# Performance work log

Measured on AMD Instinct MI355X. Metric: run time of the kernel, lower is better.

## Reference

```python
import jax, jax.numpy as jnp
import numpy as np

D_MODEL = 1024
NUM_HEADS = 16
D_K = D_MODEL // NUM_HEADS


def setup_inputs() -> dict:
    key = jax.random.key(0)
    ks = jax.random.split(key, 5)
    s = 1.0 / np.sqrt(D_MODEL)
    return {
        "x": jax.random.normal(ks[0], (2, 2048, D_MODEL), dtype=jnp.float32),
        "Wq": jax.random.normal(ks[1], (D_MODEL, D_MODEL), dtype=jnp.float32) * s,
        "bq": jnp.zeros((D_MODEL,), dtype=jnp.float32),
        "Wk": jax.random.normal(ks[2], (D_MODEL, D_MODEL), dtype=jnp.float32) * s,
        "bk": jnp.zeros((D_MODEL,), dtype=jnp.float32),
        "Wv": jax.random.normal(ks[3], (D_MODEL, D_MODEL), dtype=jnp.float32) * s,
        "bv": jnp.zeros((D_MODEL,), dtype=jnp.float32),
        "Wo": jax.random.normal(ks[4], (D_MODEL, D_MODEL), dtype=jnp.float32) * s,
        "bo": jnp.zeros((D_MODEL,), dtype=jnp.float32),
    }


def reference(x, Wq, bq, Wk, bk, Wv, bv, Wo, bo):
    B, S, D = x.shape
    H, dk = NUM_HEADS, D_K
    Q = x @ Wq + bq  # [B, S, D]
    K = x @ Wk + bk
    V = x @ Wv + bv
    # Faithful to the torch code: plain .view(B, H, S, dk) (NO transpose),
    # i.e. heads are carved out of the flattened (S*D) dim, not the feature dim.
    Q = Q.reshape(B, H, S, dk)
    K = K.reshape(B, H, S, dk)
    V = V.reshape(B, H, S, dk)
    scores = jnp.einsum("bhqd,bhkd->bhqk", Q, K) / jnp.sqrt(jnp.float32(dk))
    attn = jax.nn.softmax(scores, axis=-1)  # [B, H, S, S]
    ctx = jnp.einsum("bhqk,bhkd->bhqd", attn, V)  # [B, H, S, dk]
    out = ctx.reshape(B, S, D) @ Wo + bo
    return out  # dropout is identity in eval mode
```

## Files before the change

kernel.cpp:

```cpp
#include <hip/hip_runtime.h>
#include <hip/hip_bf16.h>
#include <math.h>

#define D_MODEL 1024
#define SEQ     2048
#define BATCH   2
#define NHEAD   16
#define DKH     64
#define BH      (BATCH * NHEAD)

typedef unsigned short u16;
typedef unsigned int   u32;
typedef __bf16 bf16x8 __attribute__((ext_vector_type(8)));
typedef float  f32x4  __attribute__((ext_vector_type(4)));

#define MFMA16(a, b, c) __builtin_amdgcn_mfma_f32_16x16x32_bf16((a), (b), (c), 0, 0, 0)
#define AS1 __attribute__((address_space(1)))
#define AS3 __attribute__((address_space(3)))

#define QSCALE 0.18033688f

__device__ __forceinline__ u16 f2bf(float x) {
    u32 u = __float_as_uint(x);
    u += 0x7fffu + ((u >> 16) & 1u);
    return (u16)(u >> 16);
}
__device__ __forceinline__ float bf2f(u16 b) {
    return __uint_as_float(((u32)b) << 16);
}
__device__ __forceinline__ void gl16(const u16* g, void* lds) {
    __builtin_amdgcn_global_load_lds((const AS1 u32*)g, (AS3 u32*)lds, 16, 0, 0);
}

__global__ __launch_bounds__(256) void conv_all(
    const float* __restrict__ x, u16* __restrict__ Xh, int n4,
    const float* __restrict__ W0, const float* __restrict__ W1,
    const float* __restrict__ W2, const float* __restrict__ W3,
    u16* __restrict__ H0, u16* __restrict__ L0, u16* __restrict__ H1, u16* __restrict__ L1,
    u16* __restrict__ H2, u16* __restrict__ L2, u16* __restrict__ H3, u16* __restrict__ L3)
{
    const int t = threadIdx.x;
    if ((int)blockIdx.x < 4096) {
        int i = blockIdx.x * 256 + t;
        if (i >= n4) return;
        float4 v = reinterpret_cast<const float4*>(x)[i];
        uint2 H;
        H.x = f2bf(v.x) | ((u32)f2bf(v.y) << 16);
        H.y = f2bf(v.z) | ((u32)f2bf(v.w) << 16);
        reinterpret_cast<uint2*>(Xh)[i] = H;
        return;
    }
    int id = blockIdx.x - 4096;
    int bx = id & 15, by = (id >> 4) & 15, bz = id >> 8;
    const float* W; u16 *Ht, *Lt;
    if (bz == 0)      { W = W0; Ht = H0; Lt = L0; }
    else if (bz == 1) { W = W1; Ht = H1; Lt = L1; }
    else if (bz == 2) { W = W2; Ht = H2; Lt = L2; }
    else              { W = W3; Ht = H3; Lt = L3; }

    __shared__ float T[64][65];
    const int n0 = bx * 64, k0 = by * 64;
    #pragma unroll
    for (int i = 0; i < 4; ++i) {
        int f = t + i * 256;
        int kr = f >> 4, ns = (f & 15) * 4;
        float4 v = *reinterpret_cast<const float4*>(&W[(size_t)(k0 + kr) * D_MODEL + n0 + ns]);
        T[kr][ns + 0] = v.x; T[kr][ns + 1] = v.y; T[kr][ns + 2] = v.z; T[kr][ns + 3] = v.w;
    }
    __syncthreads();
    #pragma unroll
    for (int i = 0; i < 4; ++i) {
        int f = t + i * 256;
        int nr = f >> 4, ks = (f & 15) * 4;
        u16 hh[4], ll[4];
        #pragma unroll
        for (int j = 0; j < 4; ++j) {
            float xv = T[ks + j][nr];
            u16 hb = f2bf(xv);
            hh[j] = hb;
            ll[j] = f2bf(xv - bf2f(hb));
        }
        uint2 H, L;
        H.x = hh[0] | ((u32)hh[1] << 16); H.y = hh[2] | ((u32)hh[3] << 16);
        L.x = ll[0] | ((u32)ll[1] << 16); L.y = ll[2] | ((u32)ll[3] << 16);
        size_t o = (size_t)(n0 + nr) * D_MODEL + k0 + ks;
        *reinterpret_cast<uint2*>(&Ht[o]) = H;
        if (bz == 3)
            *reinterpret_cast<uint2*>(&Lt[o]) = L;
    }
}

__global__ __launch_bounds__(256, 2) void gemm_qkv(
    const u16* __restrict__ AhG,
    const u16* __restrict__ Bqh, const u16* __restrict__ Bkh, const u16* __restrict__ Bvh,
    const float* __restrict__ bq, const float* __restrict__ bk, const float* __restrict__ bv,
    u16* __restrict__ Qb, u16* __restrict__ Kb, u16* __restrict__ Vb)
{
    constexpr int K = D_MODEL, N = D_MODEL;
    __shared__ u16 LB[2][10240];

    const int tid  = threadIdx.x;
    const int wv   = tid >> 6;
    const int lane = tid & 63;
    const int quad = lane >> 4;
    const int l16  = lane & 15;
    const int wm   = wv & 1, wn = wv >> 1;
    const int brow = blockIdx.y * 128, bcol = blockIdx.x * 64;

    const u16* ptrs[4] = { AhG, Bqh, Bkh, Bvh };
    const int abase[4] = { 0, 8192, 12288, 16384 };
    const u16* sp[5];
    int sldb[5];
    #pragma unroll
    for (int j = 0; j < 5; ++j) {
        int a, cc;
        if (j < 3)      { int c = wv * 3 + j; if (c < 8) { a = 0; cc = c; } else { a = 1; cc = c - 8; } }
        else if (j == 3){ a = 2; cc = wv; }
        else            { a = 3; cc = wv; }
        int row  = cc * 16 + (lane >> 2);
        int gseg = (lane & 3) ^ ((lane >> 3) & 3);
        int rbase = (a == 0) ? brow : bcol;
        sp[j]   = ptrs[a] + (size_t)(rbase + row) * K + gseg * 8;
        sldb[j] = abase[a] + cc * 1024;
    }

    int aro[4], bro[2];
    #pragma unroll
    for (int i = 0; i < 4; ++i) {
        int mr = wm * 64 + i * 16 + l16;
        aro[i] = mr * 64 + ((quad ^ ((mr >> 1) & 3)) * 16);
    }
    #pragma unroll
    for (int i = 0; i < 2; ++i) {
        int nr = wn * 32 + i * 16 + l16;
        bro[i] = nr * 64 + ((quad ^ ((nr >> 1) & 3)) * 16);
    }

    f32x4 acc[3][4][2] = {};

    auto mm = [&](int m, bf16x8 (&ah)[4], bf16x8 b0, bf16x8 b1) {
        __builtin_amdgcn_s_setprio(1);
        #pragma unroll
        for (int mi = 0; mi < 4; ++mi) {
            f32x4 c0 = acc[m][mi][0], c1 = acc[m][mi][1];
            c0 = MFMA16(ah[mi], b0, c0);
            c1 = MFMA16(ah[mi], b1, c1);
            acc[m][mi][0] = c0; acc[m][mi][1] = c1;
        }
        __builtin_amdgcn_s_setprio(0);
    };

    #pragma unroll
    for (int j = 0; j < 5; ++j)
        gl16(sp[j], (char*)LB[0] + sldb[j]);

    for (int it = 0; it < K / 32 - 1; ++it) {
        const int cur = it & 1, nx = cur ^ 1;
        const int k1 = (it + 1) * 32;
        bf16x8 ah[4], b0, b1;

        asm volatile("s_waitcnt vmcnt(2)" ::: "memory");
        __builtin_amdgcn_s_barrier();
        #pragma unroll
        for (int i = 0; i < 4; ++i)
            ah[i] = *reinterpret_cast<const bf16x8*>((const char*)LB[cur] + aro[i]);
        b0 = *reinterpret_cast<const bf16x8*>((const char*)LB[cur] + 8192 + bro[0]);
        b1 = *reinterpret_cast<const bf16x8*>((const char*)LB[cur] + 8192 + bro[1]);
        gl16(sp[0] + k1, (char*)LB[nx] + sldb[0]);
        gl16(sp[1] + k1, (char*)LB[nx] + sldb[1]);
        gl16(sp[2] + k1, (char*)LB[nx] + sldb[2]);
        mm(0, ah, b0, b1);

        asm volatile("s_waitcnt vmcnt(4)" ::: "memory");
        __builtin_amdgcn_s_barrier();
        b0 = *reinterpret_cast<const bf16x8*>((const char*)LB[cur] + 12288 + bro[0]);
        b1 = *reinterpret_cast<const bf16x8*>((const char*)LB[cur] + 12288 + bro[1]);
        gl16(sp[3] + k1, (char*)LB[nx] + sldb[3]);
        mm(1, ah, b0, b1);

        asm volatile("s_waitcnt vmcnt(4)" ::: "memory");
        __builtin_amdgcn_s_barrier();
        b0 = *reinterpret_cast<const bf16x8*>((const char*)LB[cur] + 16384 + bro[0]);
        b1 = *reinterpret_cast<const bf16x8*>((const char*)LB[cur] + 16384 + bro[1]);
        gl16(sp[4] + k1, (char*)LB[nx] + sldb[4]);
        mm(2, ah, b0, b1);
    }

    {
        const int cur = (K / 32 - 1) & 1;
        bf16x8 ah[4], b0, b1;

        asm volatile("s_waitcnt vmcnt(2)" ::: "memory");
        __builtin_amdgcn_s_barrier();
        #pragma unroll
        for (int i = 0; i < 4; ++i)
            ah[i] = *reinterpret_cast<const bf16x8*>((const char*)LB[cur] + aro[i]);
        b0 = *reinterpret_cast<const bf16x8*>((const char*)LB[cur] + 8192 + bro[0]);
        b1 = *reinterpret_cast<const bf16x8*>((const char*)LB[cur] + 8192 + bro[1]);
        mm(0, ah, b0, b1);

        asm volatile("s_waitcnt vmcnt(1)" ::: "memory");
        __builtin_amdgcn_s_barrier();
        b0 = *reinterpret_cast<const bf16x8*>((const char*)LB[cur] + 12288 + bro[0]);
        b1 = *reinterpret_cast<const bf16x8*>((const char*)LB[cur] + 12288 + bro[1]);
        mm(1, ah, b0, b1);

        asm volatile("s_waitcnt vmcnt(0)" ::: "memory");
        __builtin_amdgcn_s_barrier();
        b0 = *reinterpret_cast<const bf16x8*>((const char*)LB[cur] + 16384 + bro[0]);
        b1 = *reinterpret_cast<const bf16x8*>((const char*)LB[cur] + 16384 + bro[1]);
        mm(2, ah, b0, b1);
    }

    #pragma unroll
    for (int m = 0; m < 3; ++m) {
        const float* bias = (m == 0) ? bq : (m == 1) ? bk : bv;
        u16* out = (m == 0) ? Qb : (m == 1) ? Kb : Vb;
        const float sc = (m == 0) ? QSCALE : 1.0f;
        #pragma unroll
        for (int mi = 0; mi < 4; ++mi) {
            #pragma unroll
            for (int ni = 0; ni < 2; ++ni) {
                int col = bcol + wn * 32 + ni * 16 + l16;
                float bvv = bias[col];
                #pragma unroll
                for (int r = 0; r < 4; ++r) {
                    int row = brow + wm * 64 + mi * 16 + quad * 4 + r;
                    out[(size_t)row * N + col] = f2bf((acc[m][mi][ni][r] + bvv) * sc);
                }
            }
        }
    }
}

__global__ __launch_bounds__(256, 2) void gemm_oproj(
    const u16* __restrict__ AhG, const u16* __restrict__ Bh, const u16* __restrict__ Bl,
    const float* __restrict__ bias, float* __restrict__ Cf)
{
    constexpr int K = D_MODEL, N = D_MODEL;
    __shared__ u16 LB[2][8192];

    const int tid  = threadIdx.x;
    const int wv   = tid >> 6;
    const int lane = tid & 63;
    const int quad = lane >> 4;
    const int l16  = lane & 15;
    const int wm   = wv & 1, wn = wv >> 1;
    const int brow = blockIdx.y * 128, bcol = blockIdx.x * 64;

    const u16* ptrs[3] = { AhG, Bh, Bl };
    const int abase[3] = { 0, 8192, 12288 };
    const u16* sp[4];
    int sldb[4];
    #pragma unroll
    for (int j = 0; j < 4; ++j) {
        int a, cc;
        if (j < 3) { int c = wv * 3 + j;  a = (c < 8) ? 0 : 1; cc = (c < 8) ? c : (c - 8); }
        else       { a = 2; cc = wv; }
        int row  = cc * 16 + (lane >> 2);
        int gseg = (lane & 3) ^ ((lane >> 3) & 3);
        int rbase = (a == 0) ? brow : bcol;
        sp[j]   = ptrs[a] + (size_t)(rbase + row) * K + gseg * 8;
        sldb[j] = abase[a] + cc * 1024;
    }

    int aro[4], bro[2];
    #pragma unroll
    for (int i = 0; i < 4; ++i) {
        int mr = wm * 64 + i * 16 + l16;
        aro[i] = mr * 64 + ((quad ^ ((mr >> 1) & 3)) * 16);
    }
    #pragma unroll
    for (int i = 0; i < 2; ++i) {
        int nr = wn * 32 + i * 16 + l16;
        bro[i] = nr * 64 + ((quad ^ ((nr >> 1) & 3)) * 16);
    }

    f32x4 acc[4][2] = {};

    auto mmc = [&](bf16x8 (&ah)[4], bf16x8 b0, bf16x8 b1) {
        __builtin_amdgcn_s_setprio(1);
        #pragma unroll
        for (int mi = 0; mi < 4; ++mi) {
            f32x4 c0 = acc[mi][0], c1 = acc[mi][1];
            c0 = MFMA16(ah[mi], b0, c0);
            c1 = MFMA16(ah[mi], b1, c1);
            acc[mi][0] = c0; acc[mi][1] = c1;
        }
        __builtin_amdgcn_s_setprio(0);
    };

    #pragma unroll
    for (int j = 0; j < 4; ++j)
        gl16(sp[j], (char*)LB[0] + sldb[j]);

    for (int it = 0; it < K / 32 - 1; ++it) {
        const int cur = it & 1, nx = cur ^ 1;
        const int k1 = (it + 1) * 32;
        bf16x8 ah[4], b0, b1;

        asm volatile("s_waitcnt vmcnt(1)" ::: "memory");
        __builtin_amdgcn_s_barrier();
        #pragma unroll
        for (int i = 0; i < 4; ++i)
            ah[i] = *reinterpret_cast<const bf16x8*>((const char*)LB[cur] + aro[i]);
        b0 = *reinterpret_cast<const bf16x8*>((const char*)LB[cur] + 8192 + bro[0]);
        b1 = *reinterpret_cast<const bf16x8*>((const char*)LB[cur] + 8192 + bro[1]);
        gl16(sp[0] + k1, (char*)LB[nx] + sldb[0]);
        gl16(sp[1] + k1, (char*)LB[nx] + sldb[1]);
        gl16(sp[2] + k1, (char*)LB[nx] + sldb[2]);
        mmc(ah, b0, b1);

        asm volatile("s_waitcnt vmcnt(3)" ::: "memory");
        __builtin_amdgcn_s_barrier();
        b0 = *reinterpret_cast<const bf16x8*>((const char*)LB[cur] + 12288 + bro[0]);
        b1 = *reinterpret_cast<const bf16x8*>((const char*)LB[cur] + 12288 + bro[1]);
        gl16(sp[3] + k1, (char*)LB[nx] + sldb[3]);
        mmc(ah, b0, b1);
    }

    {
        const int cur = (K / 32 - 1) & 1;
        bf16x8 ah[4], b0, b1;

        asm volatile("s_waitcnt vmcnt(1)" ::: "memory");
        __builtin_amdgcn_s_barrier();
        #pragma unroll
        for (int i = 0; i < 4; ++i)
            ah[i] = *reinterpret_cast<const bf16x8*>((const char*)LB[cur] + aro[i]);
        b0 = *reinterpret_cast<const bf16x8*>((const char*)LB[cur] + 8192 + bro[0]);
        b1 = *reinterpret_cast<const bf16x8*>((const char*)LB[cur] + 8192 + bro[1]);
        mmc(ah, b0, b1);

        asm volatile("s_waitcnt vmcnt(0)" ::: "memory");
        __builtin_amdgcn_s_barrier();
        b0 = *reinterpret_cast<const bf16x8*>((const char*)LB[cur] + 12288 + bro[0]);
        b1 = *reinterpret_cast<const bf16x8*>((const char*)LB[cur] + 12288 + bro[1]);
        mmc(ah, b0, b1);
    }

    #pragma unroll
    for (int mi = 0; mi < 4; ++mi) {
        #pragma unroll
        for (int ni = 0; ni < 2; ++ni) {
            int col = bcol + wn * 32 + ni * 16 + l16;
            float bvv = bias[col];
            #pragma unroll
            for (int r = 0; r < 4; ++r) {
                int row = brow + wm * 64 + mi * 16 + quad * 4 + r;
                Cf[(size_t)row * N + col] = acc[mi][ni][r] + bvv;
            }
        }
    }
}

__global__ __launch_bounds__(256) void v_transpose(
    const u16* __restrict__ V, u16* __restrict__ Vt)
{
    __shared__ u16 T[64][72];
    const int bh = blockIdx.y, st = blockIdx.x;
    const u16* src = V + ((size_t)bh * SEQ + (size_t)st * 64) * 64;
    const int t = threadIdx.x;
    #pragma unroll
    for (int i = 0; i < 2; ++i) {
        int c  = t + i * 256;
        int s  = c >> 3;
        int d0 = (c & 7) * 8;
        uint4 v = reinterpret_cast<const uint4*>(src)[c];
        u16 e[8];
        e[0] = (u16)(v.x & 0xffff); e[1] = (u16)(v.x >> 16);
        e[2] = (u16)(v.y & 0xffff); e[3] = (u16)(v.y >> 16);
        e[4] = (u16)(v.z & 0xffff); e[5] = (u16)(v.z >> 16);
        e[6] = (u16)(v.w & 0xffff); e[7] = (u16)(v.w >> 16);
        #pragma unroll
        for (int j = 0; j < 8; ++j) T[d0 + j][s] = e[j];
    }
    __syncthreads();
    const int d = t >> 2, seg = t & 3;
    u16* dst = Vt + (size_t)bh * 64 * SEQ + (size_t)d * SEQ + st * 64;
    #pragma unroll
    for (int gg = 0; gg < 2; ++gg) {
        int g = seg * 2 + gg;
        u32 r0 = *reinterpret_cast<const u32*>(&T[d][2 * g]);
        u32 r1 = *reinterpret_cast<const u32*>(&T[d][2 * g + 16]);
        u32 r2 = *reinterpret_cast<const u32*>(&T[d][2 * g + 32]);
        u32 r3 = *reinterpret_cast<const u32*>(&T[d][2 * g + 48]);
        uint4 w;
        w.x = (r0 & 0xffffu) | (r1 << 16);
        w.y = (r2 & 0xffffu) | (r3 << 16);
        w.z = (r0 >> 16) | (r1 & 0xffff0000u);
        w.w = (r2 >> 16) | (r3 & 0xffff0000u);
        *reinterpret_cast<uint4*>(&dst[8 * g]) = w;
    }
}

__global__ __launch_bounds__(512, 4) void attn_mfma(
    const u16* __restrict__ Qb_g, const u16* __restrict__ Kb_g,
    const u16* __restrict__ Vt_g, u16* __restrict__ Ch_g)
{
    __shared__ u16 KVS[3][8192];
    __shared__ u16 Pb [128 * 72];

    const int tid  = threadIdx.x;
    const int wv   = tid >> 6;
    const int lane = tid & 63;
    const int quad = lane >> 4;
    const int l16  = lane & 15;
    const int id   = blockIdx.x;
    const int bh   = id & 31;
    const int qt   = id >> 5;
    const int qrow = wv * 16;

    const size_t qbase = ((size_t)bh * SEQ + (size_t)qt * 128) * 64;
    const size_t kbh   = (size_t)bh * SEQ * 64;
    const size_t vtbh  = (size_t)bh * 64 * SEQ;

    bf16x8 qf[2];
    #pragma unroll
    for (int ks = 0; ks < 2; ++ks) {
        size_t o = qbase + (size_t)(qrow + l16) * 64 + ks * 32 + quad * 8;
        qf[ks] = *reinterpret_cast<const bf16x8*>(Qb_g + o);
    }

    const u16* sp[2];
    size_t sstep[2];
    int sldb[2];
    #pragma unroll
    for (int j = 0; j < 2; ++j) {
        int c   = wv * 2 + j;
        int arr = c >> 3, cc = c & 7;
        int row = cc * 8 + (lane >> 3);
        int sg  = (lane & 7) ^ (row & 7);
        if (arr == 0) { sp[j] = Kb_g + kbh + (size_t)row * 64 + sg * 8;   sstep[j] = 4096; }
        else          { sp[j] = Vt_g + vtbh + (size_t)row * SEQ + sg * 8; sstep[j] = 64; }
        sldb[j] = arr * 8192 + cc * 1024;
    }

    int fro[4][2];
    #pragma unroll
    for (int t = 0; t < 4; ++t)
        #pragma unroll
        for (int ks = 0; ks < 2; ++ks)
            fro[t][ks] = (t * 16 + l16) * 128 + (((ks * 4 + quad) ^ (l16 & 7)) * 16);

    bf16x8 onesv;
    #pragma unroll
    for (int i = 0; i < 8; ++i) onesv[i] = (__bf16)1.0f;

    f32x4 oacc[4] = {};
    f32x4 lsum = {};

    auto S_step = [&](int bufidx, f32x4 (&sacc)[4]) {
        const char* kb = (const char*)KVS[bufidx];
        #pragma unroll
        for (int t4 = 0; t4 < 4; ++t4) {
            bf16x8 kh0 = *reinterpret_cast<const bf16x8*>(kb + fro[t4][0]);
            bf16x8 kh1 = *reinterpret_cast<const bf16x8*>(kb + fro[t4][1]);
            f32x4 a = sacc[t4];
            a = MFMA16(qf[0], kh0, a);
            a = MFMA16(qf[1], kh1, a);
            sacc[t4] = a;
        }
    };

    auto PV_step = [&](int bufidx) {
        const char* vb = (const char*)KVS[bufidx] + 8192;
        bf16x8 bvf[4][2];
        #pragma unroll
        for (int dt = 0; dt < 4; ++dt) {
            bvf[dt][0] = *reinterpret_cast<const bf16x8*>(vb + fro[dt][0]);
            bvf[dt][1] = *reinterpret_cast<const bf16x8*>(vb + fro[dt][1]);
        }
        bf16x8 ap[2];
        #pragma unroll
        for (int ks = 0; ks < 2; ++ks)
            ap[ks] = *reinterpret_cast<const bf16x8*>(
                &Pb[(qrow + l16) * 72 + ks * 32 + quad * 8]);
        #pragma unroll
        for (int dt = 0; dt < 4; ++dt) {
            oacc[dt] = MFMA16(ap[0], bvf[dt][0], oacc[dt]);
            oacc[dt] = MFMA16(ap[1], bvf[dt][1], oacc[dt]);
        }
        lsum = MFMA16(ap[0], onesv, lsum);
        lsum = MFMA16(ap[1], onesv, lsum);
    };

    auto EXP2_step = [&](f32x4 (&sacc)[4]) {
        const int rowb = qrow + quad * 4;
        #pragma unroll
        for (int r = 0; r < 4; ++r) {
            u32 u0 = __float_as_uint(__builtin_amdgcn_exp2f(sacc[0][r]));
            u32 u1 = __float_as_uint(__builtin_amdgcn_exp2f(sacc[1][r]));
            u32 u2 = __float_as_uint(__builtin_amdgcn_exp2f(sacc[2][r]));
            u32 u3 = __float_as_uint(__builtin_amdgcn_exp2f(sacc[3][r]));
            uint2 w;
            w.x = (u0 >> 16) | (u1 & 0xffff0000u);
            w.y = (u2 >> 16) | (u3 & 0xffff0000u);
            *reinterpret_cast<uint2*>(&Pb[(rowb + r) * 72 + l16 * 4]) = w;
        }
    };

    #pragma unroll
    for (int j = 0; j < 2; ++j)
        gl16(sp[j], (char*)KVS[0] + sldb[j]);

    {
        __syncthreads();
        #pragma unroll
        for (int j = 0; j < 2; ++j)
            gl16(sp[j] + sstep[j], (char*)KVS[1] + sldb[j]);
        f32x4 sacc[4] = {};
        __builtin_amdgcn_s_setprio(1);
        S_step(0, sacc);
        __builtin_amdgcn_s_setprio(0);
        EXP2_step(sacc);
    }

    int cur = 1, prv = 0, nxt = 2;
    for (int kt = 1; kt < SEQ / 64; ++kt) {
        __syncthreads();
        if (kt + 1 < SEQ / 64) {
            #pragma unroll
            for (int j = 0; j < 2; ++j)
                gl16(sp[j] + (size_t)(kt + 1) * sstep[j], (char*)KVS[nxt] + sldb[j]);
        }

        f32x4 sacc[4] = {};
        __builtin_amdgcn_s_setprio(1);
        S_step(cur, sacc);
        PV_step(prv);
        __builtin_amdgcn_s_setprio(0);
        EXP2_step(sacc);

        prv = cur; cur = nxt; nxt = (nxt == 2) ? 0 : nxt + 1;
    }

    __builtin_amdgcn_s_setprio(1);
    PV_step(prv);
    __builtin_amdgcn_s_setprio(0);

    u16* Oh = Ch_g + qbase;
    float inv[4];
    #pragma unroll
    for (int r = 0; r < 4; ++r) inv[r] = 1.0f / lsum[r];
    #pragma unroll
    for (int dt = 0; dt < 4; ++dt)
        #pragma unroll
        for (int r = 0; r < 4; ++r) {
            int row = qrow + quad * 4 + r;
            Oh[(size_t)row * 64 + dt * 16 + l16] = f2bf(oacc[dt][r] * inv[r]);
        }
}

extern "C" void kernel_launch(void* const* d_in, const int* in_sizes, int n_in,
                              void* d_out, int out_size, void* d_ws, size_t ws_size,
                              hipStream_t stream)
{
    const float* x  = (const float*)d_in[0];
    const float* Wq = (const float*)d_in[1];
    const float* bq = (const float*)d_in[2];
    const float* Wk = (const float*)d_in[3];
    const float* bk = (const float*)d_in[4];
    const float* Wv = (const float*)d_in[5];
    const float* bv = (const float*)d_in[6];
    const float* Wo = (const float*)d_in[7];
    const float* bo = (const float*)d_in[8];
    float* out = (float*)d_out;

    const int M = BATCH * SEQ;
    const int N = D_MODEL;
    const size_t NE = (size_t)M * N;
    const size_t NW = (size_t)N * N;

    u16* w16 = (u16*)d_ws;
    u16* Xh   = w16;
    u16* Qb   = Xh   + NE;
    u16* Kb   = Qb   + NE;
    u16* Vb   = Kb   + NE;
    u16* Vtb  = Vb   + NE;
    u16* Ctxh = Vtb  + NE;
    u16* WTqh = Ctxh + NE;
    u16* WTql = WTqh + NW;
    u16* WTkh = WTql + NW;
    u16* WTkl = WTkh + NW;
    u16* WTvh = WTkl + NW;
    u16* WTvl = WTvh + NW;
    u16* WToh = WTvl + NW;
    u16* WTol = WToh + NW;

    conv_all<<<dim3(4096 + 1024), dim3(256), 0, stream>>>(
        x, Xh, (int)(NE / 4),
        Wq, Wk, Wv, Wo, WTqh, WTql, WTkh, WTkl, WTvh, WTvl, WToh, WTol);

    gemm_qkv<<<dim3(N / 64, M / 128), dim3(256), 0, stream>>>(
        Xh, WTqh, WTkh, WTvh, bq, bk, bv, Qb, Kb, Vb);

    v_transpose<<<dim3(SEQ / 64, BH), dim3(256), 0, stream>>>(Vb, Vtb);

    attn_mfma<<<dim3((SEQ / 128) * BH), dim3(512), 0, stream>>>(Qb, Kb, Vtb, Ctxh);

    gemm_oproj<<<dim3(N / 64, M / 128), dim3(256), 0, stream>>>(
        Ctxh, WToh, WTol, bo, out);
}
```

Measured before the change: 190.8 us.

## Give each attention wave two 16-row query subtiles to reuse K/V fragments

The attention kernel now runs 256 threads (4 waves) per block instead of 512, and each wave handles 32 query rows as two 16-row subtiles. Each K and V fragment read from LDS feeds twice as many MFMAs, and each thread issues four async global-to-LDS copies per tile instead of two. This cuts LDS read traffic per MFMA and the number of waves contending at barriers. In exchange, per-wave register pressure roughly doubles for accumulators and Q fragments, and there are fewer waves per block to hide latency.

```diff
diff --git a/kernel.cpp b/kernel.cpp
--- a/kernel.cpp
+++ b/kernel.cpp
@@ -394,7 +394,7 @@
     }
 }
 
-__global__ __launch_bounds__(512, 4) void attn_mfma(
+__global__ __launch_bounds__(256, 2) void attn_mfma(
     const u16* __restrict__ Qb_g, const u16* __restrict__ Kb_g,
     const u16* __restrict__ Vt_g, u16* __restrict__ Ch_g)
 {
@@ -409,25 +409,27 @@
     const int id   = blockIdx.x;
     const int bh   = id & 31;
     const int qt   = id >> 5;
-    const int qrow = wv * 16;
+    const int qrow = wv * 32;
 
     const size_t qbase = ((size_t)bh * SEQ + (size_t)qt * 128) * 64;
     const size_t kbh   = (size_t)bh * SEQ * 64;
     const size_t vtbh  = (size_t)bh * 64 * SEQ;
 
-    bf16x8 qf[2];
-    #pragma unroll
-    for (int ks = 0; ks < 2; ++ks) {
-        size_t o = qbase + (size_t)(qrow + l16) * 64 + ks * 32 + quad * 8;
-        qf[ks] = *reinterpret_cast<const bf16x8*>(Qb_g + o);
-    }
-
-    const u16* sp[2];
-    size_t sstep[2];
-    int sldb[2];
-    #pragma unroll
-    for (int j = 0; j < 2; ++j) {
-        int c   = wv * 2 + j;
+    bf16x8 qf[2][2];
+    #pragma unroll
+    for (int sub = 0; sub < 2; ++sub)
+        #pragma unroll
+        for (int ks = 0; ks < 2; ++ks) {
+            size_t o = qbase + (size_t)(qrow + sub * 16 + l16) * 64 + ks * 32 + quad * 8;
+            qf[sub][ks] = *reinterpret_cast<const bf16x8*>(Qb_g + o);
+        }
+
+    const u16* sp[4];
+    size_t sstep[4];
+    int sldb[4];
+    #pragma unroll
+    for (int j = 0; j < 4; ++j) {
+        int c   = wv * 4 + j;
         int arr = c >> 3, cc = c & 7;
         int row = cc * 8 + (lane >> 3);
         int sg  = (lane & 7) ^ (row & 7);
@@ -447,19 +449,22 @@
     #pragma unroll
     for (int i = 0; i < 8; ++i) onesv[i] = (__bf16)1.0f;
 
-    f32x4 oacc[4] = {};
-    f32x4 lsum = {};
-
-    auto S_step = [&](int bufidx, f32x4 (&sacc)[4]) {
+    f32x4 oacc[2][4] = {};
+    f32x4 lsum[2] = {};
+
+    auto S_step = [&](int bufidx, f32x4 (&sacc)[2][4]) {
         const char* kb = (const char*)KVS[bufidx];
         #pragma unroll
         for (int t4 = 0; t4 < 4; ++t4) {
             bf16x8 kh0 = *reinterpret_cast<const bf16x8*>(kb + fro[t4][0]);
             bf16x8 kh1 = *reinterpret_cast<const bf16x8*>(kb + fro[t4][1]);
-            f32x4 a = sacc[t4];
-            a = MFMA16(qf[0], kh0, a);
-            a = MFMA16(qf[1], kh1, a);
-            sacc[t4] = a;
+            #pragma unroll
+            for (int sub = 0; sub < 2; ++sub) {
+                f32x4 a = sacc[sub][t4];
+                a = MFMA16(qf[sub][0], kh0, a);
+                a = MFMA16(qf[sub][1], kh1, a);
+                sacc[sub][t4] = a;
+            }
         }
     };
 
@@ -471,45 +476,51 @@
             bvf[dt][0] = *reinterpret_cast<const bf16x8*>(vb + fro[dt][0]);
             bvf[dt][1] = *reinterpret_cast<const bf16x8*>(vb + fro[dt][1]);
         }
-        bf16x8 ap[2];
-        #pragma unroll
-        for (int ks = 0; ks < 2; ++ks)
-            ap[ks] = *reinterpret_cast<const bf16x8*>(
-                &Pb[(qrow + l16) * 72 + ks * 32 + quad * 8]);
-        #pragma unroll
-        for (int dt = 0; dt < 4; ++dt) {
-            oacc[dt] = MFMA16(ap[0], bvf[dt][0], oacc[dt]);
-            oacc[dt] = MFMA16(ap[1], bvf[dt][1], oacc[dt]);
-        }
-        lsum = MFMA16(ap[0], onesv, lsum);
-        lsum = MFMA16(ap[1], onesv, lsum);
+        #pragma unroll
+        for (int sub = 0; sub < 2; ++sub) {
+            bf16x8 ap[2];
+            #pragma unroll
+            for (int ks = 0; ks < 2; ++ks)
+                ap[ks] = *reinterpret_cast<const bf16x8*>(
+                    &Pb[(qrow + sub * 16 + l16) * 72 + ks * 32 + quad * 8]);
+            #pragma unroll
+            for (int dt = 0; dt < 4; ++dt) {
+                oacc[sub][dt] = MFMA16(ap[0], bvf[dt][0], oacc[sub][dt]);
+                oacc[sub][dt] = MFMA16(ap[1], bvf[dt][1], oacc[sub][dt]);
+            }
+            lsum[sub] = MFMA16(ap[0], onesv, lsum[sub]);
+            lsum[sub] = MFMA16(ap[1], onesv, lsum[sub]);
+        }
     };
 
-    auto EXP2_step = [&](f32x4 (&sacc)[4]) {
-        const int rowb = qrow + quad * 4;
-        #pragma unroll
-        for (int r = 0; r < 4; ++r) {
-            u32 u0 = __float_as_uint(__builtin_amdgcn_exp2f(sacc[0][r]));
-            u32 u1 = __float_as_uint(__builtin_amdgcn_exp2f(sacc[1][r]));
-            u32 u2 = __float_as_uint(__builtin_amdgcn_exp2f(sacc[2][r]));
-            u32 u3 = __float_as_uint(__builtin_amdgcn_exp2f(sacc[3][r]));
-            uint2 w;
-            w.x = (u0 >> 16) | (u1 & 0xffff0000u);
-            w.y = (u2 >> 16) | (u3 & 0xffff0000u);
-            *reinterpret_cast<uint2*>(&Pb[(rowb + r) * 72 + l16 * 4]) = w;
+    auto EXP2_step = [&](f32x4 (&sacc)[2][4]) {
+        #pragma unroll
+        for (int sub = 0; sub < 2; ++sub) {
+            const int rowb = qrow + sub * 16 + quad * 4;
+            #pragma unroll
+            for (int r = 0; r < 4; ++r) {
+                u32 u0 = __float_as_uint(__builtin_amdgcn_exp2f(sacc[sub][0][r]));
+                u32 u1 = __float_as_uint(__builtin_amdgcn_exp2f(sacc[sub][1][r]));
+                u32 u2 = __float_as_uint(__builtin_amdgcn_exp2f(sacc[sub][2][r]));
+                u32 u3 = __float_as_uint(__builtin_amdgcn_exp2f(sacc[sub][3][r]));
+                uint2 w;
+                w.x = (u0 >> 16) | (u1 & 0xffff0000u);
+                w.y = (u2 >> 16) | (u3 & 0xffff0000u);
+                *reinterpret_cast<uint2*>(&Pb[(rowb + r) * 72 + l16 * 4]) = w;
+            }
         }
     };
 
     #pragma unroll
-    for (int j = 0; j < 2; ++j)
+    for (int j = 0; j < 4; ++j)
         gl16(sp[j], (char*)KVS[0] + sldb[j]);
 
     {
         __syncthreads();
         #pragma unroll
-        for (int j = 0; j < 2; ++j)
+        for (int j = 0; j < 4; ++j)
             gl16(sp[j] + sstep[j], (char*)KVS[1] + sldb[j]);
-        f32x4 sacc[4] = {};
+        f32x4 sacc[2][4] = {};
         __builtin_amdgcn_s_setprio(1);
         S_step(0, sacc);
         __builtin_amdgcn_s_setprio(0);
@@ -521,11 +532,11 @@
         __syncthreads();
         if (kt + 1 < SEQ / 64) {
             #pragma unroll
-            for (int j = 0; j < 2; ++j)
+            for (int j = 0; j < 4; ++j)
                 gl16(sp[j] + (size_t)(kt + 1) * sstep[j], (char*)KVS[nxt] + sldb[j]);
         }
 
-        f32x4 sacc[4] = {};
+        f32x4 sacc[2][4] = {};
         __builtin_amdgcn_s_setprio(1);
         S_step(cur, sacc);
         PV_step(prv);
@@ -540,16 +551,19 @@
     __builtin_amdgcn_s_setprio(0);
 
     u16* Oh = Ch_g + qbase;
-    float inv[4];
-    #pragma unroll
-    for (int r = 0; r < 4; ++r) inv[r] = 1.0f / lsum[r];
-    #pragma unroll
-    for (int dt = 0; dt < 4; ++dt)
-        #pragma unroll
-        for (int r = 0; r < 4; ++r) {
-            int row = qrow + quad * 4 + r;
-            Oh[(size_t)row * 64 + dt * 16 + l16] = f2bf(oacc[dt][r] * inv[r]);
-        }
+    #pragma unroll
+    for (int sub = 0; sub < 2; ++sub) {
+        float inv[4];
+        #pragma unroll
+        for (int r = 0; r < 4; ++r) inv[r] = 1.0f / lsum[sub][r];
+        #pragma unroll
+        for (int dt = 0; dt < 4; ++dt)
+            #pragma unroll
+            for (int r = 0; r < 4; ++r) {
+                int row = qrow + sub * 16 + quad * 4 + r;
+                Oh[(size_t)row * 64 + dt * 16 + l16] = f2bf(oacc[sub][dt][r] * inv[r]);
+            }
+    }
 }
 
 extern "C" void kernel_launch(void* const* d_in, const int* in_sizes, int n_in,
@@ -597,7 +611,7 @@
 
     v_transpose<<<dim3(SEQ / 64, BH), dim3(256), 0, stream>>>(Vb, Vtb);
 
-    attn_mfma<<<dim3((SEQ / 128) * BH), dim3(512), 0, stream>>>(Qb, Kb, Vtb, Ctxh);
+    attn_mfma<<<dim3((SEQ / 128) * BH), dim3(256), 0, stream>>>(Qb, Kb, Vtb, Ctxh);
 
     gemm_oproj<<<dim3(N / 64, M / 128), dim3(256), 0, stream>>>(
         Ctxh, WToh, WTol, bo, out);
```

New measurement: 188.7 us. About the same (-1.1%).

## Deepen QKV GEMM prefetch to two stages and batch LDS reads per iteration

Applied to the files above, without the earlier changes.

The QKV projection GEMM loop now keeps two K-tiles in flight instead of one. It issues loads for tile it+2 into the buffer that was just drained to registers. All A and Q/K/V B fragments are read from LDS up front, then a single barrier releases the buffer. This replaces three barrier-separated phases per iteration with one. The three MFMA groups then run back-to-back under raised priority, aiming to cut barrier count and hide global latency better, at the cost of more live registers.

```diff
diff --git a/kernel.cpp b/kernel.cpp
--- a/kernel.cpp
+++ b/kernel.cpp
@@ -139,7 +139,6 @@
     f32x4 acc[3][4][2] = {};
 
     auto mm = [&](int m, bf16x8 (&ah)[4], bf16x8 b0, bf16x8 b1) {
-        __builtin_amdgcn_s_setprio(1);
         #pragma unroll
         for (int mi = 0; mi < 4; ++mi) {
             f32x4 c0 = acc[m][mi][0], c1 = acc[m][mi][1];
@@ -147,69 +146,69 @@
             c1 = MFMA16(ah[mi], b1, c1);
             acc[m][mi][0] = c0; acc[m][mi][1] = c1;
         }
-        __builtin_amdgcn_s_setprio(0);
     };
 
     #pragma unroll
     for (int j = 0; j < 5; ++j)
         gl16(sp[j], (char*)LB[0] + sldb[j]);
+    #pragma unroll
+    for (int j = 0; j < 5; ++j)
+        gl16(sp[j] + 32, (char*)LB[1] + sldb[j]);
 
     for (int it = 0; it < K / 32 - 1; ++it) {
-        const int cur = it & 1, nx = cur ^ 1;
-        const int k1 = (it + 1) * 32;
-        bf16x8 ah[4], b0, b1;
-
-        asm volatile("s_waitcnt vmcnt(2)" ::: "memory");
+        const int cur = it & 1;
+
+        asm volatile("s_waitcnt vmcnt(5)" ::: "memory");
         __builtin_amdgcn_s_barrier();
+
+        bf16x8 ah[4], q0, q1, k0, k1, v0, v1;
         #pragma unroll
         for (int i = 0; i < 4; ++i)
             ah[i] = *reinterpret_cast<const bf16x8*>((const char*)LB[cur] + aro[i]);
-        b0 = *reinterpret_cast<const bf16x8*>((const char*)LB[cur] + 8192 + bro[0]);
-        b1 = *reinterpret_cast<const bf16x8*>((const char*)LB[cur] + 8192 + bro[1]);
-        gl16(sp[0] + k1, (char*)LB[nx] + sldb[0]);
-        gl16(sp[1] + k1, (char*)LB[nx] + sldb[1]);
-        gl16(sp[2] + k1, (char*)LB[nx] + sldb[2]);
-        mm(0, ah, b0, b1);
-
-        asm volatile("s_waitcnt vmcnt(4)" ::: "memory");
+        q0 = *reinterpret_cast<const bf16x8*>((const char*)LB[cur] + 8192 + bro[0]);
+        q1 = *reinterpret_cast<const bf16x8*>((const char*)LB[cur] + 8192 + bro[1]);
+        k0 = *reinterpret_cast<const bf16x8*>((const char*)LB[cur] + 12288 + bro[0]);
+        k1 = *reinterpret_cast<const bf16x8*>((const char*)LB[cur] + 12288 + bro[1]);
+        v0 = *reinterpret_cast<const bf16x8*>((const char*)LB[cur] + 16384 + bro[0]);
+        v1 = *reinterpret_cast<const bf16x8*>((const char*)LB[cur] + 16384 + bro[1]);
+
+        asm volatile("s_waitcnt lgkmcnt(0)" ::: "memory");
+        __builtin_amdgcn_sched_barrier(0);
         __builtin_amdgcn_s_barrier();
-        b0 = *reinterpret_cast<const bf16x8*>((const char*)LB[cur] + 12288 + bro[0]);
-        b1 = *reinterpret_cast<const bf16x8*>((const char*)LB[cur] + 12288 + bro[1]);
-        gl16(sp[3] + k1, (char*)LB[nx] + sldb[3]);
-        mm(1, ah, b0, b1);
-
-        asm volatile("s_waitcnt vmcnt(4)" ::: "memory");
-        __builtin_amdgcn_s_barrier();
-        b0 = *reinterpret_cast<const bf16x8*>((const char*)LB[cur] + 16384 + bro[0]);
-        b1 = *reinterpret_cast<const bf16x8*>((const char*)LB[cur] + 16384 + bro[1]);
-        gl16(sp[4] + k1, (char*)LB[nx] + sldb[4]);
-        mm(2, ah, b0, b1);
+
+        if (it + 2 < K / 32) {
+            const int k2 = (it + 2) * 32;
+            #pragma unroll
+            for (int j = 0; j < 5; ++j)
+                gl16(sp[j] + k2, (char*)LB[cur] + sldb[j]);
+        }
+
+        __builtin_amdgcn_s_setprio(1);
+        mm(0, ah, q0, q1);
+        mm(1, ah, k0, k1);
+        mm(2, ah, v0, v1);
+        __builtin_amdgcn_s_setprio(0);
     }
 
     {
         const int cur = (K / 32 - 1) & 1;
-        bf16x8 ah[4], b0, b1;
-
-        asm volatile("s_waitcnt vmcnt(2)" ::: "memory");
+        asm volatile("s_waitcnt vmcnt(0)" ::: "memory");
         __builtin_amdgcn_s_barrier();
+        bf16x8 ah[4], q0, q1, k0, k1, v0, v1;
         #pragma unroll
         for (int i = 0; i < 4; ++i)
             ah[i] = *reinterpret_cast<const bf16x8*>((const char*)LB[cur] + aro[i]);
-        b0 = *reinterpret_cast<const bf16x8*>((const char*)LB[cur] + 8192 + bro[0]);
-        b1 = *reinterpret_cast<const bf16x8*>((const char*)LB[cur] + 8192 + bro[1]);
-        mm(0, ah, b0, b1);
-
-        asm volatile("s_waitcnt vmcnt(1)" ::: "memory");
-        __builtin_amdgcn_s_barrier();
-        b0 = *reinterpret_cast<const bf16x8*>((const char*)LB[cur] + 12288 + bro[0]);
-        b1 = *reinterpret_cast<const bf16x8*>((const char*)LB[cur] + 12288 + bro[1]);
-        mm(1, ah, b0, b1);
-
-        asm volatile("s_waitcnt vmcnt(0)" ::: "memory");
-        __builtin_amdgcn_s_barrier();
-        b0 = *reinterpret_cast<const bf16x8*>((const char*)LB[cur] + 16384 + bro[0]);
-        b1 = *reinterpret_cast<const bf16x8*>((const char*)LB[cur] + 16384 + bro[1]);
-        mm(2, ah, b0, b1);
+        q0 = *reinterpret_cast<const bf16x8*>((const char*)LB[cur] + 8192 + bro[0]);
+        q1 = *reinterpret_cast<const bf16x8*>((const char*)LB[cur] + 8192 + bro[1]);
+        k0 = *reinterpret_cast<const bf16x8*>((const char*)LB[cur] + 12288 + bro[0]);
+        k1 = *reinterpret_cast<const bf16x8*>((const char*)LB[cur] + 12288 + bro[1]);
+        v0 = *reinterpret_cast<const bf16x8*>((const char*)LB[cur] + 16384 + bro[0]);
+        v1 = *reinterpret_cast<const bf16x8*>((const char*)LB[cur] + 16384 + bro[1]);
+        __builtin_amdgcn_s_setprio(1);
+        mm(0, ah, q0, q1);
+        mm(1, ah, k0, k1);
+        mm(2, ah, v0, v1);
+        __builtin_amdgcn_s_setprio(0);
     }
 
     #pragma unroll
```

Result: no change. 189.3 us (-0.8%).
